# Kernel optimization log

Hardware: AMD Instinct MI355X
Metric: run time of the kernel (lower is better)

The kernel has to match this reference:

```python
import jax, jax.numpy as jnp
import numpy as np

ALPHA, GAMMA, THRESHOLD, NUM_CLASSES = 0.5, 1.5, 0.5, 21
EPS8, EPS7 = 1e-8, 1e-7


def corner_to_center(b):
    w = b[..., 2] - b[..., 0]
    h = b[..., 3] - b[..., 1]
    cx = b[..., 0] + w / 2
    cy = b[..., 1] + h / 2
    return jnp.stack([cx, cy, w, h], axis=-1)


def box_iou(b1, b2):
    # b1: [P,4], b2: [M,4] -> [P,M]
    area1 = (b1[:, 2] - b1[:, 0]) * (b1[:, 3] - b1[:, 1])
    area2 = (b2[:, 2] - b2[:, 0]) * (b2[:, 3] - b2[:, 1])
    lt = jnp.maximum(b1[:, None, :2], b2[None, :, :2])
    rb = jnp.minimum(b1[:, None, 2:], b2[None, :, 2:])
    wh = jnp.clip(rb - lt, 0)
    inter = wh[..., 0] * wh[..., 1]
    return inter / (area1[:, None] + area2[None, :] - inter)


def encode_boxes(matched, dbox):
    g = corner_to_center(matched)
    d = corner_to_center(dbox)
    ex = (g[..., 0] - d[..., 0]) / (d[..., 2] + EPS8)
    ey = (g[..., 1] - d[..., 1]) / (d[..., 3] + EPS8)
    ew = jnp.log(g[..., 2] / (d[..., 2] + EPS8) + EPS8)
    eh = jnp.log(g[..., 3] / (d[..., 3] + EPS8) + EPS8)
    return jnp.stack([ex, ey, ew, eh], axis=-1)


def decode_boxes(loc, dbox):
    d = corner_to_center(dbox)
    cx = loc[..., 0] * d[..., 2] + d[..., 0]
    cy = loc[..., 1] * d[..., 3] + d[..., 1]
    w = jnp.exp(loc[..., 2]) * d[..., 2]
    h = jnp.exp(loc[..., 3]) * d[..., 3]
    return jnp.stack([cx - w / 2, cy - h / 2, cx + w / 2, cy + h / 2], axis=-1)


def giou_loss(pred, tgt):
    inter_min = jnp.maximum(pred[..., :2], tgt[..., :2])
    inter_max = jnp.minimum(pred[..., 2:], tgt[..., 2:])
    inter_wh = jnp.clip(inter_max - inter_min, 0)
    inter = inter_wh[..., 0] * inter_wh[..., 1]
    pa = (pred[..., 2] - pred[..., 0]) * (pred[..., 3] - pred[..., 1])
    ta = (tgt[..., 2] - tgt[..., 0]) * (tgt[..., 3] - tgt[..., 1])
    union = pa + ta - inter
    iou = inter / (union + EPS7)
    encl_min = jnp.minimum(pred[..., :2], tgt[..., :2])
    encl_max = jnp.maximum(pred[..., 2:], tgt[..., 2:])
    encl_wh = jnp.clip(encl_max - encl_min, 0)
    encl = encl_wh[..., 0] * encl_wh[..., 1]
    giou = iou - (encl - union) / (encl + EPS7)
    return 1.0 - giou


def _match_one(truths, labels, dbox):
    # truths: [M,4], labels: [M], dbox: [P,4]
    M = truths.shape[0]
    overlaps = box_iou(dbox, truths)               # [P,M]
    bt_ov = overlaps.max(axis=1)                   # [P]
    bt_idx = overlaps.argmax(axis=1)               # [P]
    bp_idx = overlaps.argmax(axis=0)               # [M] best prior per GT
    # force-match each GT to its best prior
    bt_idx = bt_idx.at[bp_idx].set(jnp.arange(M))
    bt_ov = bt_ov.at[bp_idx].set(2.0)
    matches = truths[bt_idx]                       # [P,4]
    mlabels = jnp.where(bt_ov < THRESHOLD, 0, labels[bt_idx])
    loc_t = encode_boxes(matches, dbox)
    return loc_t, mlabels


def focal_loss(pred, target):
    # pred: [N,C], target: [N]
    logp = jax.nn.log_softmax(pred, axis=-1)
    ce = -jnp.take_along_axis(logp, target[:, None], axis=1)[:, 0]
    p_t = jnp.exp(-ce)
    return ALPHA * (1.0 - p_t) ** GAMMA * ce


def setup_inputs() -> dict:
    key = jax.random.key(0)
    k1, k2, k3, k4, k5, k6, k7 = jax.random.split(key, 7)
    B, P, M, C = 64, 24564, 50, 21
    # valid corner-format boxes: min + positive wh
    d_min = jax.random.uniform(k1, (P, 2)) * 0.8
    d_wh = 0.05 + jax.random.uniform(k2, (P, 2)) * 0.2
    default_boxes = jnp.concatenate([d_min, d_min + d_wh], axis=1)
    g_min = jax.random.uniform(k3, (B, M, 2)) * 0.8
    g_wh = 0.05 + jax.random.uniform(k4, (B, M, 2)) * 0.2
    gt_boxes = jnp.concatenate([g_min, g_min + g_wh], axis=2)
    loc_preds = jax.random.normal(k5, (B, P, 4)) * 0.1
    conf_preds = jax.random.normal(k6, (B, P, C))
    gt_labels = jax.random.randint(k7, (B, M), 1, C)
    return {"loc_preds": loc_preds, "conf_preds": conf_preds,
            "default_boxes": default_boxes, "gt_boxes": gt_boxes,
            "gt_labels": gt_labels}


def reference(loc_preds, conf_preds, default_boxes, gt_boxes, gt_labels):
    B, P, _ = loc_preds.shape
    loc_t, conf_t = jax.vmap(_match_one, in_axes=(0, 0, None))(gt_boxes, gt_labels, default_boxes)
    pos = conf_t > 0                                   # [B,P]
    num_pos = pos.sum()
    denom = jnp.maximum(num_pos, 1).astype(loc_preds.dtype)
    # localization: decode preds and targets against anchors, GIoU on positives
    decoded_pred = decode_boxes(loc_preds, default_boxes[None])
    decoded_tgt = decode_boxes(loc_t, default_boxes[None])
    gl = giou_loss(decoded_pred, decoded_tgt)          # [B,P]
    loc_loss = jnp.sum(jnp.where(pos, gl, 0.0)) / denom
    # classification: focal loss over all anchors
    fl = focal_loss(conf_preds.reshape(-1, conf_preds.shape[-1]), conf_t.reshape(-1))
    conf_loss = fl.sum() / denom
    total = loc_loss + conf_loss
    return jnp.where(num_pos == 0, 0.0, total)
```

## Files before the change

kernel.cpp:

```cpp
#include <hip/hip_runtime.h>
#include <cstdint>
#include <cstddef>

#define F_ALPHA 0.5f
#define THRESH  0.5f
#define EPS8    1e-8f
#define EPS7    1e-7f
#define MAXM    64
#define CCLS    21
#define GGRP    4

__global__ __launch_bounds__(256)
void bp_kernel(const float4* __restrict__ dbox,
               const float4* __restrict__ gt,
               unsigned* __restrict__ bp,
               float* __restrict__ garea,
               int P, int M)
{
    __shared__ unsigned long long wkey[GGRP][4];

    const int b  = blockIdx.y;
    const int m0 = blockIdx.x * GGRP;
    const int t  = threadIdx.x;
    const int w  = t >> 6, lane = t & 63;

    float4 gb[GGRP]; float ga[GGRP];
    #pragma unroll
    for (int g = 0; g < GGRP; g++) {
        int m = min(m0 + g, M - 1);
        float4 gg = gt[(size_t)b * M + m];
        gb[g] = gg;
        ga[g] = (gg.z - gg.x) * (gg.w - gg.y);
    }

    float    bestv[GGRP];
    unsigned bestp[GGRP];
    #pragma unroll
    for (int g = 0; g < GGRP; g++) { bestv[g] = 0.f; bestp[g] = 0u; }

    for (int p = t; p < P; p += 256) {
        float4 d = dbox[p];
        float darea = (d.z - d.x) * (d.w - d.y);
        #pragma unroll
        for (int g = 0; g < GGRP; g++) {
            float4 gg = gb[g];
            float lx = fmaxf(d.x, gg.x), ly = fmaxf(d.y, gg.y);
            float rx = fminf(d.z, gg.z), ry = fminf(d.w, gg.w);
            float iw = fmaxf(rx - lx, 0.f), ih = fmaxf(ry - ly, 0.f);
            float inter = iw * ih;
            float iou = inter * __builtin_amdgcn_rcpf(darea + ga[g] - inter);
            if (iou > bestv[g]) { bestv[g] = iou; bestp[g] = (unsigned)p; }
        }
    }

    #pragma unroll
    for (int g = 0; g < GGRP; g++) {
        unsigned long long k =
            ((unsigned long long)__float_as_uint(bestv[g]) << 32)
            | (unsigned long long)(0xFFFFFFFFu - bestp[g]);
        #pragma unroll
        for (int o = 1; o < 64; o <<= 1) {
            unsigned long long k2 = __shfl_xor(k, o, 64);
            if (k2 > k) k = k2;
        }
        if (lane == 0) wkey[g][w] = k;
    }
    __syncthreads();
    if (t < GGRP) {
        unsigned long long k0 = wkey[t][0], k1 = wkey[t][1];
        unsigned long long k2 = wkey[t][2], k3 = wkey[t][3];
        unsigned long long ka = (k0 > k1) ? k0 : k1;
        unsigned long long kb = (k2 > k3) ? k2 : k3;
        unsigned long long k  = (ka > kb) ? ka : kb;
        int m = m0 + t;
        if (m < M) {
            bp[(size_t)b * M + m] = 0xFFFFFFFFu - (unsigned)(k & 0xFFFFFFFFull);
            float4 gg = gt[(size_t)b * M + m];
            garea[(size_t)b * M + m] = (gg.z - gg.x) * (gg.w - gg.y);
        }
    }
}

__global__ __launch_bounds__(256, 6)
void loss_kernel(const float4* __restrict__ locp,
                 const float*  __restrict__ conf,
                 const float4* __restrict__ dbox,
                 const float4* __restrict__ gt,
                 const float*  __restrict__ garea,
                 const int*    __restrict__ gtl,
                 const unsigned* __restrict__ bp,
                 double* __restrict__ partS,
                 int*    __restrict__ partC,
                 int P, int M)
{
    __shared__ float    scf[256 * CCLS];
    __shared__ float4   tb[MAXM];
    __shared__ int      tl[MAXM];
    __shared__ int      ovr[256];
    __shared__ double   sv[4];
    __shared__ int      sc[4];

    const int t = threadIdx.x;
    const int b = blockIdx.y;
    const int p0 = blockIdx.x * 256;
    const int p = p0 + t;
    const bool valid = (p < P);

    ovr[t] = -1;
    if (t < M) {
        tb[t] = gt[(size_t)b * M + t];
        tl[t] = gtl[(size_t)b * M + t];
    }

    const int cnt = min(256, P - p0);
    const int nf = cnt * CCLS;
    const float* src = conf + ((size_t)b * P + p0) * CCLS;
    {
        const int n4 = nf >> 2;
        const float4* s4 = (const float4*)src;
        float4* d4 = (float4*)scf;
        for (int i = t; i < n4; i += 256) d4[i] = s4[i];
        for (int i = (n4 << 2) + t; i < nf; i += 256) scf[i] = src[i];
    }
    __syncthreads();

    if (t < M) {
        unsigned q = bp[(size_t)b * M + t] - (unsigned)p0;
        if (q < 256u) atomicMax(&ovr[q], t);
    }

    float4 d = make_float4(0.f, 0.f, 0.f, 0.f);
    float bi = -1.0f, bd = 1.0f;
    int   bm = 0;
    if (valid) {
        d = dbox[p];
        const float darea = (d.z - d.x) * (d.w - d.y);
        const float4* gtb = gt + (size_t)b * M;
        const float*  gab = garea + (size_t)b * M;
        const int Mpad = (M + 3) & ~3;
        for (int m0 = 0; m0 < Mpad; m0 += 4) {
            #pragma unroll
            for (int k = 0; k < 4; k++) {
                int mc = min(m0 + k, M - 1);
                float4 g = gtb[mc];
                float ta = gab[mc];
                float lx = fmaxf(d.x, g.x), ly = fmaxf(d.y, g.y);
                float rx = fminf(d.z, g.z), ry = fminf(d.w, g.w);
                float iw = fmaxf(rx - lx, 0.f), ih = fmaxf(ry - ly, 0.f);
                float inter = iw * ih;
                float den = darea + ta - inter;
                if (inter * bd > bi * den) { bi = inter; bd = den; bm = m0 + k; }
            }
        }
    }
    __syncthreads();

    double acc = 0.0;
    int cnt_pos = 0;
    if (valid) {
        int  idx = bm;
        bool pos = (bi >= THRESH * bd);
        int j = ovr[t];
        if (j >= 0) { idx = j; pos = true; }
        int lbl = pos ? tl[idx] : 0;

        float xv[CCLS];
        const float* x = scf + t * CCLS;
        #pragma unroll
        for (int c = 0; c < CCLS; c++) xv[c] = x[c];
        float xl = scf[t * CCLS + lbl];
        float mx = xv[0];
        #pragma unroll
        for (int c = 1; c < CCLS; c++) mx = fmaxf(mx, xv[c]);
        float sum = 0.f;
        #pragma unroll
        for (int c = 0; c < CCLS; c++) sum += expf(xv[c] - mx);
        float ce = (mx + logf(sum)) - xl;
        float pt = expf(-ce);
        float om = 1.f - pt;
        acc = (double)(F_ALPHA * om * sqrtf(om) * ce);

        if (pos) {
            cnt_pos = 1;
            float dw = d.z - d.x, dh = d.w - d.y;
            float dcx = d.x + dw * 0.5f, dcy = d.y + dh * 0.5f;
            float4 g = tb[idx];
            float gw = g.z - g.x, gh = g.w - g.y;
            float gcx = g.x + gw * 0.5f, gcy = g.y + gh * 0.5f;
            float ex = (gcx - dcx) / (dw + EPS8);
            float ey = (gcy - dcy) / (dh + EPS8);
            float ew = logf(gw / (dw + EPS8) + EPS8);
            float eh = logf(gh / (dh + EPS8) + EPS8);
            float tcx = ex * dw + dcx, tcy = ey * dh + dcy;
            float tw = expf(ew) * dw,  th = expf(eh) * dh;
            float t0 = tcx - tw * 0.5f, t1 = tcy - th * 0.5f;
            float t2 = tcx + tw * 0.5f, t3 = tcy + th * 0.5f;
            float4 l = locp[(size_t)b * P + p];
            float pcx = l.x * dw + dcx, pcy = l.y * dh + dcy;
            float pw = expf(l.z) * dw,  ph = expf(l.w) * dh;
            float q0 = pcx - pw * 0.5f, q1 = pcy - ph * 0.5f;
            float q2 = pcx + pw * 0.5f, q3 = pcy + ph * 0.5f;
            float ix0 = fmaxf(q0, t0), iy0 = fmaxf(q1, t1);
            float ix1 = fminf(q2, t2), iy1 = fminf(q3, t3);
            float iw = fmaxf(ix1 - ix0, 0.f), ih = fmaxf(iy1 - iy0, 0.f);
            float inter = iw * ih;
            float pa = (q2 - q0) * (q3 - q1);
            float ta = (t2 - t0) * (t3 - t1);
            float uni = pa + ta - inter;
            float iou = inter / (uni + EPS7);
            float e0 = fminf(q0, t0), e1 = fminf(q1, t1);
            float e2 = fmaxf(q2, t2), e3 = fmaxf(q3, t3);
            float ewd = fmaxf(e2 - e0, 0.f), ehd = fmaxf(e3 - e1, 0.f);
            float encl = ewd * ehd;
            float giou = iou - (encl - uni) / (encl + EPS7);
            acc += (double)(1.f - giou);
        }
    }

    for (int o = 32; o > 0; o >>= 1) {
        acc += __shfl_down(acc, o, 64);
        cnt_pos += __shfl_down(cnt_pos, o, 64);
    }
    int w = t >> 6, lane = t & 63;
    if (lane == 0) { sv[w] = acc; sc[w] = cnt_pos; }
    __syncthreads();
    if (t == 0) {
        int slot = blockIdx.y * gridDim.x + blockIdx.x;
        partS[slot] = sv[0] + sv[1] + sv[2] + sv[3];
        partC[slot] = sc[0] + sc[1] + sc[2] + sc[3];
    }
}

__global__ __launch_bounds__(256)
void final_kernel(const double* __restrict__ partS,
                  const int*    __restrict__ partC,
                  float* __restrict__ out, int n)
{
    __shared__ double sv[4];
    __shared__ long long sc[4];
    const int t = threadIdx.x;
    double a = 0.0; long long c = 0;
    for (int i = t; i < n; i += 256) { a += partS[i]; c += partC[i]; }
    for (int o = 32; o > 0; o >>= 1) {
        a += __shfl_down(a, o, 64);
        c += __shfl_down(c, o, 64);
    }
    int w = t >> 6, lane = t & 63;
    if (lane == 0) { sv[w] = a; sc[w] = c; }
    __syncthreads();
    if (t == 0) {
        double s = sv[0] + sv[1] + sv[2] + sv[3];
        long long np = sc[0] + sc[1] + sc[2] + sc[3];
        out[0] = (np == 0) ? 0.0f : (float)(s / (double)np);
    }
}

extern "C" void kernel_launch(void* const* d_in, const int* in_sizes, int n_in,
                              void* d_out, int out_size, void* d_ws, size_t ws_size,
                              hipStream_t stream)
{
    const float* locp = (const float*)d_in[0];
    const float* conf = (const float*)d_in[1];
    const float* dbox = (const float*)d_in[2];
    const float* gt   = (const float*)d_in[3];
    const int*   gtl  = (const int*)d_in[4];

    const int P  = in_sizes[2] / 4;
    const long long BP = (long long)in_sizes[0] / 4;
    const int B  = (int)(BP / P);
    const int M  = in_sizes[4] / B;

    const int nblk = (P + 255) / 256;
    const int nPart = nblk * B;

    char* ws = (char*)d_ws;
    unsigned* bp = (unsigned*)ws;
    size_t off = ((size_t)B * M * 4 + 15) & ~(size_t)15;
    float* garea = (float*)(ws + off);
    off += ((size_t)B * M * 4 + 15) & ~(size_t)15;
    double* partS = (double*)(ws + off);
    off += (size_t)nPart * 8;
    int* partC = (int*)(ws + off);

    dim3 gridBP((M + GGRP - 1) / GGRP, B);
    dim3 grid(nblk, B);
    bp_kernel<<<gridBP, 256, 0, stream>>>((const float4*)dbox, (const float4*)gt,
                                          bp, garea, P, M);
    loss_kernel<<<grid, 256, 0, stream>>>((const float4*)locp, conf,
                                          (const float4*)dbox, (const float4*)gt,
                                          garea, gtl, bp, partS, partC, P, M);
    final_kernel<<<1, 256, 0, stream>>>(partS, partC, (float*)d_out, nPart);
}
```

Baseline: 302.2 us.

## Stage confidence tile in two halves to halve LDS and raise occupancy

The loss kernel now loads the 256x21 confidence tile into shared memory in two 128-row phases, which halves LDS use, and raises the launch-bounds occupancy hint from 6 to 8. The IoU matching loop now runs before the conf staging, and the gt-box shared-memory copy is replaced by a direct global load of the matched box. The softmax uses exp2/log2 builtins in place of expf/logf. In exchange there are extra __syncthreads barriers, half the threads sit idle during each phase, and the staged load no longer overlaps the matching loop.

```diff
diff --git a/kernel.cpp b/kernel.cpp
--- a/kernel.cpp
+++ b/kernel.cpp
@@ -9,6 +9,8 @@
 #define MAXM    64
 #define CCLS    21
 #define GGRP    4
+#define LOG2E   1.4426950408889634f
+#define LN2     0.6931471805599453f
 
 __global__ __launch_bounds__(256)
 void bp_kernel(const float4* __restrict__ dbox,
@@ -81,7 +83,7 @@
     }
 }
 
-__global__ __launch_bounds__(256, 6)
+__global__ __launch_bounds__(256, 8)
 void loss_kernel(const float4* __restrict__ locp,
                  const float*  __restrict__ conf,
                  const float4* __restrict__ dbox,
@@ -93,8 +95,7 @@
                  int*    __restrict__ partC,
                  int P, int M)
 {
-    __shared__ float    scf[256 * CCLS];
-    __shared__ float4   tb[MAXM];
+    __shared__ float    scf[128 * CCLS];
     __shared__ int      tl[MAXM];
     __shared__ int      ovr[256];
     __shared__ double   sv[4];
@@ -107,21 +108,7 @@
     const bool valid = (p < P);
 
     ovr[t] = -1;
-    if (t < M) {
-        tb[t] = gt[(size_t)b * M + t];
-        tl[t] = gtl[(size_t)b * M + t];
-    }
-
-    const int cnt = min(256, P - p0);
-    const int nf = cnt * CCLS;
-    const float* src = conf + ((size_t)b * P + p0) * CCLS;
-    {
-        const int n4 = nf >> 2;
-        const float4* s4 = (const float4*)src;
-        float4* d4 = (float4*)scf;
-        for (int i = t; i < n4; i += 256) d4[i] = s4[i];
-        for (int i = (n4 << 2) + t; i < nf; i += 256) scf[i] = src[i];
-    }
+    if (t < M) tl[t] = gtl[(size_t)b * M + t];
     __syncthreads();
 
     if (t < M) {
@@ -129,92 +116,115 @@
         if (q < 256u) atomicMax(&ovr[q], t);
     }
 
-    float4 d = make_float4(0.f, 0.f, 0.f, 0.f);
+    const int pc = valid ? p : (P - 1);
+    const float4 d = dbox[pc];
+    const float darea = (d.z - d.x) * (d.w - d.y);
+    const float4* gtb = gt + (size_t)b * M;
+    const float*  gab = garea + (size_t)b * M;
     float bi = -1.0f, bd = 1.0f;
     int   bm = 0;
-    if (valid) {
-        d = dbox[p];
-        const float darea = (d.z - d.x) * (d.w - d.y);
-        const float4* gtb = gt + (size_t)b * M;
-        const float*  gab = garea + (size_t)b * M;
-        const int Mpad = (M + 3) & ~3;
-        for (int m0 = 0; m0 < Mpad; m0 += 4) {
-            #pragma unroll
-            for (int k = 0; k < 4; k++) {
-                int mc = min(m0 + k, M - 1);
-                float4 g = gtb[mc];
-                float ta = gab[mc];
-                float lx = fmaxf(d.x, g.x), ly = fmaxf(d.y, g.y);
-                float rx = fminf(d.z, g.z), ry = fminf(d.w, g.w);
-                float iw = fmaxf(rx - lx, 0.f), ih = fmaxf(ry - ly, 0.f);
-                float inter = iw * ih;
-                float den = darea + ta - inter;
-                if (inter * bd > bi * den) { bi = inter; bd = den; bm = m0 + k; }
-            }
-        }
-    }
-    __syncthreads();
+    const int Mpad = (M + 3) & ~3;
+    for (int m0 = 0; m0 < Mpad; m0 += 4) {
+        #pragma unroll
+        for (int k = 0; k < 4; k++) {
+            int mc = min(m0 + k, M - 1);
+            float4 g = gtb[mc];
+            float ta = gab[mc];
+            float lx = fmaxf(d.x, g.x), ly = fmaxf(d.y, g.y);
+            float rx = fminf(d.z, g.z), ry = fminf(d.w, g.w);
+            float iw = fmaxf(rx - lx, 0.f), ih = fmaxf(ry - ly, 0.f);
+            float inter = iw * ih;
+            float den = darea + ta - inter;
+            if (inter * bd > bi * den) { bi = inter; bd = den; bm = m0 + k; }
+        }
+    }
+    __syncthreads();
+
+    int  idx = bm;
+    bool pos = (bi >= THRESH * bd);
+    { int j = ovr[t]; if (j >= 0) { idx = j; pos = true; } }
+    const int lbl = pos ? tl[idx] : 0;
+
+    const int cnt = min(256, P - p0);
+    const float* src = conf + ((size_t)b * P + p0) * CCLS;
 
     double acc = 0.0;
     int cnt_pos = 0;
-    if (valid) {
-        int  idx = bm;
-        bool pos = (bi >= THRESH * bd);
-        int j = ovr[t];
-        if (j >= 0) { idx = j; pos = true; }
-        int lbl = pos ? tl[idx] : 0;
-
-        float xv[CCLS];
-        const float* x = scf + t * CCLS;
-        #pragma unroll
-        for (int c = 0; c < CCLS; c++) xv[c] = x[c];
-        float xl = scf[t * CCLS + lbl];
-        float mx = xv[0];
-        #pragma unroll
-        for (int c = 1; c < CCLS; c++) mx = fmaxf(mx, xv[c]);
-        float sum = 0.f;
-        #pragma unroll
-        for (int c = 0; c < CCLS; c++) sum += expf(xv[c] - mx);
-        float ce = (mx + logf(sum)) - xl;
-        float pt = expf(-ce);
-        float om = 1.f - pt;
-        acc = (double)(F_ALPHA * om * sqrtf(om) * ce);
-
-        if (pos) {
-            cnt_pos = 1;
-            float dw = d.z - d.x, dh = d.w - d.y;
-            float dcx = d.x + dw * 0.5f, dcy = d.y + dh * 0.5f;
-            float4 g = tb[idx];
-            float gw = g.z - g.x, gh = g.w - g.y;
-            float gcx = g.x + gw * 0.5f, gcy = g.y + gh * 0.5f;
-            float ex = (gcx - dcx) / (dw + EPS8);
-            float ey = (gcy - dcy) / (dh + EPS8);
-            float ew = logf(gw / (dw + EPS8) + EPS8);
-            float eh = logf(gh / (dh + EPS8) + EPS8);
-            float tcx = ex * dw + dcx, tcy = ey * dh + dcy;
-            float tw = expf(ew) * dw,  th = expf(eh) * dh;
-            float t0 = tcx - tw * 0.5f, t1 = tcy - th * 0.5f;
-            float t2 = tcx + tw * 0.5f, t3 = tcy + th * 0.5f;
-            float4 l = locp[(size_t)b * P + p];
-            float pcx = l.x * dw + dcx, pcy = l.y * dh + dcy;
-            float pw = expf(l.z) * dw,  ph = expf(l.w) * dh;
-            float q0 = pcx - pw * 0.5f, q1 = pcy - ph * 0.5f;
-            float q2 = pcx + pw * 0.5f, q3 = pcy + ph * 0.5f;
-            float ix0 = fmaxf(q0, t0), iy0 = fmaxf(q1, t1);
-            float ix1 = fminf(q2, t2), iy1 = fminf(q3, t3);
-            float iw = fmaxf(ix1 - ix0, 0.f), ih = fmaxf(iy1 - iy0, 0.f);
-            float inter = iw * ih;
-            float pa = (q2 - q0) * (q3 - q1);
-            float ta = (t2 - t0) * (t3 - t1);
-            float uni = pa + ta - inter;
-            float iou = inter / (uni + EPS7);
-            float e0 = fminf(q0, t0), e1 = fminf(q1, t1);
-            float e2 = fmaxf(q2, t2), e3 = fmaxf(q3, t3);
-            float ewd = fmaxf(e2 - e0, 0.f), ehd = fmaxf(e3 - e1, 0.f);
-            float encl = ewd * ehd;
-            float giou = iou - (encl - uni) / (encl + EPS7);
-            acc += (double)(1.f - giou);
-        }
+
+    #pragma unroll 1
+    for (int ph = 0; ph < 2; ph++) {
+        const int r0 = ph << 7;
+        const int rows = min(128, cnt - r0);
+        if (rows > 0) {
+            const int nf = rows * CCLS;
+            const float* s = src + r0 * CCLS;
+            if (((uintptr_t)s & 15) == 0) {
+                const int n4 = nf >> 2;
+                const float4* s4 = (const float4*)s;
+                float4* d4 = (float4*)scf;
+                for (int i = t; i < n4; i += 256) d4[i] = s4[i];
+                for (int i = (n4 << 2) + t; i < nf; i += 256) scf[i] = s[i];
+            } else {
+                for (int i = t; i < nf; i += 256) scf[i] = s[i];
+            }
+        }
+        __syncthreads();
+        if (valid && (t >> 7) == ph) {
+            const int rl = t & 127;
+            float xv[CCLS];
+            const float* x = scf + rl * CCLS;
+            #pragma unroll
+            for (int c = 0; c < CCLS; c++) xv[c] = x[c];
+            float xl = scf[rl * CCLS + lbl];
+            float mx = xv[0];
+            #pragma unroll
+            for (int c = 1; c < CCLS; c++) mx = fmaxf(mx, xv[c]);
+            float sum = 0.f;
+            #pragma unroll
+            for (int c = 0; c < CCLS; c++)
+                sum += __builtin_exp2f((xv[c] - mx) * LOG2E);
+            float ce = (mx + __builtin_log2f(sum) * LN2) - xl;
+            float pt = __builtin_exp2f(-ce * LOG2E);
+            float om = 1.f - pt;
+            acc = (double)(F_ALPHA * om * sqrtf(om) * ce);
+        }
+        __syncthreads();
+    }
+
+    if (valid && pos) {
+        cnt_pos = 1;
+        float dw = d.z - d.x, dh = d.w - d.y;
+        float dcx = d.x + dw * 0.5f, dcy = d.y + dh * 0.5f;
+        float4 g = gt[(size_t)b * M + idx];
+        float gw = g.z - g.x, gh = g.w - g.y;
+        float gcx = g.x + gw * 0.5f, gcy = g.y + gh * 0.5f;
+        float ex = (gcx - dcx) / (dw + EPS8);
+        float ey = (gcy - dcy) / (dh + EPS8);
+        float ew = logf(gw / (dw + EPS8) + EPS8);
+        float eh = logf(gh / (dh + EPS8) + EPS8);
+        float tcx = ex * dw + dcx, tcy = ey * dh + dcy;
+        float tw = expf(ew) * dw,  th = expf(eh) * dh;
+        float t0 = tcx - tw * 0.5f, t1 = tcy - th * 0.5f;
+        float t2 = tcx + tw * 0.5f, t3 = tcy + th * 0.5f;
+        float4 l = locp[(size_t)b * P + p];
+        float pcx = l.x * dw + dcx, pcy = l.y * dh + dcy;
+        float pw = expf(l.z) * dw,  ph = expf(l.w) * dh;
+        float q0 = pcx - pw * 0.5f, q1 = pcy - ph * 0.5f;
+        float q2 = pcx + pw * 0.5f, q3 = pcy + ph * 0.5f;
+        float ix0 = fmaxf(q0, t0), iy0 = fmaxf(q1, t1);
+        float ix1 = fminf(q2, t2), iy1 = fminf(q3, t3);
+        float iw = fmaxf(ix1 - ix0, 0.f), ih = fmaxf(iy1 - iy0, 0.f);
+        float inter = iw * ih;
+        float pa = (q2 - q0) * (q3 - q1);
+        float ta = (t2 - t0) * (t3 - t1);
+        float uni = pa + ta - inter;
+        float iou = inter / (uni + EPS7);
+        float e0 = fminf(q0, t0), e1 = fminf(q1, t1);
+        float e2 = fmaxf(q2, t2), e3 = fmaxf(q3, t3);
+        float ewd = fmaxf(e2 - e0, 0.f), ehd = fmaxf(e3 - e1, 0.f);
+        float encl = ewd * ehd;
+        float giou = iou - (encl - uni) / (encl + EPS7);
+        acc += (double)(1.f - giou);
     }
 
     for (int o = 32; o > 0; o >>= 1) {
```

Result: slower. 320.5 us (+6.1%).
